# Optimization experiments

Hardware: AMD Instinct MI355X
Metric: run time of the kernel (lower is better)

The kernel has to match this reference:

```python
import jax, jax.numpy as jnp
import numpy as np

# 4-bit symmetric narrow-range weight quant (Brevitas Int-WeightPerTensorFloat style)
# and 4-bit unsigned activation quant after ReLU (QuantReLU style), with
# straight-through rounding so the same code is valid for the bwd reference.

W_QMAX = 7.0    # 2**(4-1)-1, narrow range symmetric int4: [-7, 7]
A_QMAX = 15.0   # unsigned 4-bit: [0, 15]
EPS = 1e-8


def _round_ste(x):
    return x + jax.lax.stop_gradient(jnp.round(x) - x)


def quant_weight(W):
    # per-tensor scale from max abs value
    scale = jnp.max(jnp.abs(W)) / W_QMAX + EPS
    q = jnp.clip(_round_ste(W / scale), -W_QMAX, W_QMAX)
    return q * scale


def quant_relu(x, scale):
    # ReLU fused with unsigned 4-bit quant/dequant, per-tensor learned scale
    q = jnp.clip(_round_ste(jax.nn.relu(x) / scale), 0.0, A_QMAX)
    return q * scale


def setup_inputs() -> dict:
    key = jax.random.key(0)
    k = jax.random.split(key, 4)
    B = 65536
    x = jax.random.normal(k[0], (B, 28, 28), dtype=jnp.float32)
    W1 = jax.random.normal(k[1], (512, 784), dtype=jnp.float32) * 0.05
    W2 = jax.random.normal(k[2], (512, 512), dtype=jnp.float32) * 0.05
    W3 = jax.random.normal(k[3], (10, 512), dtype=jnp.float32) * 0.05
    s1 = jnp.float32(1.0)  # QuantReLU activation scales (learned params)
    s2 = jnp.float32(1.0)
    return {"x": x, "W1": W1, "W2": W2, "W3": W3, "s1": s1, "s2": s2}


def reference(x, W1, W2, W3, s1, s2):
    h = x.reshape(x.shape[0], -1)                       # flatten [B, 784]
    h = h @ quant_weight(W1).T                          # QuantLinear 784->512
    h = quant_relu(h, s1)                               # QuantReLU
    h = h @ quant_weight(W2).T                          # QuantLinear 512->512
    h = quant_relu(h, s2)                               # QuantReLU
    logits = h @ quant_weight(W3).T                     # QuantLinear 512->10
    return logits
```

## Files before the change

### kernel.cpp

```cpp
#include <hip/hip_runtime.h>
#include <hip/hip_fp16.h>

typedef _Float16 f16;
typedef _Float16 f16x4 __attribute__((ext_vector_type(4)));
typedef _Float16 f16x8 __attribute__((ext_vector_type(8)));
typedef float f32x4 __attribute__((ext_vector_type(4)));
typedef int i32x4 __attribute__((ext_vector_type(4)));

#define MFMA16(a, b, c) __builtin_amdgcn_mfma_f32_16x16x32_f16((a), (b), (c), 0, 0, 0)
#define MFMAI8(a, b, c) __builtin_amdgcn_mfma_i32_16x16x64_i8((a), (b), (c), 0, 0, 0)

#define FLAG_CAP (1024 * 1024)
#define FLAG_TOL 1e-3f

#define SBAR()   __builtin_amdgcn_s_barrier()
#define SCHEDB() __builtin_amdgcn_sched_barrier(0)

__device__ __forceinline__ void gld16(const void* g, void* l) {
    __builtin_amdgcn_global_load_lds(
        (const __attribute__((address_space(1))) unsigned int*)g,
        (__attribute__((address_space(3))) unsigned int*)l,
        16, 0, 0);
}


__global__ void k_zero(float* p, int* cnt) {
    if (threadIdx.x < 3) p[threadIdx.x] = 0.f;
    if (threadIdx.x == 3) { cnt[0] = 0; cnt[1] = 0; }
}

__global__ void k_absmax(const float* __restrict__ w, int n, float* __restrict__ out) {
    float m = 0.f;
    int stride = gridDim.x * blockDim.x;
    for (int i = blockIdx.x * blockDim.x + threadIdx.x; i < n; i += stride)
        m = fmaxf(m, fabsf(w[i]));
    #pragma unroll
    for (int o = 32; o > 0; o >>= 1) m = fmaxf(m, __shfl_down(m, o));
    __shared__ float sm[4];
    int lane = threadIdx.x & 63, wv = threadIdx.x >> 6;
    if (lane == 0) sm[wv] = m;
    __syncthreads();
    if (threadIdx.x == 0) {
        float mm = fmaxf(fmaxf(sm[0], sm[1]), fmaxf(sm[2], sm[3]));
        atomicMax((unsigned int*)out, __float_as_uint(mm));
    }
}

__global__ void k_quantw1(const float* __restrict__ w, const float* __restrict__ wmax,
                          float* __restrict__ wdq, f16* __restrict__ q1h) {
    int i = blockIdx.x * blockDim.x + threadIdx.x;
    if (i >= 512 * 832) return;
    int n = i / 832, k = i - n * 832;
    float v = 0.f;
    if (k < 784) {
        float s = wmax[0] / 7.0f + 1e-8f;
        v = rintf(w[n * 784 + k] / s);
        v = fminf(fmaxf(v, -7.f), 7.f);
        wdq[n * 784 + k] = v * s;
    }
    q1h[(size_t)n * 832 + k] = (f16)v;
}

__global__ void k_quantw2(const float* __restrict__ w, const float* __restrict__ wmax,
                          signed char* __restrict__ q, float* __restrict__ wdq, int n) {
    float s = wmax[0] / 7.0f + 1e-8f;
    int i = blockIdx.x * blockDim.x + threadIdx.x;
    if (i < n) {
        float v = rintf(w[i] / s);
        v = fminf(fmaxf(v, -7.f), 7.f);
        q[i] = (signed char)v;
        if (wdq) wdq[i] = v * s;
    }
}

__global__ void k_quantw3(const float* __restrict__ w, const float* __restrict__ wmax,
                          signed char* __restrict__ q) {
    float s = wmax[0] / 7.0f + 1e-8f;
    int i = blockIdx.x * blockDim.x + threadIdx.x;
    if (i < 16 * 512) {
        float v = 0.f;
        if (i < 10 * 512) {
            v = rintf(w[i] / s);
            v = fminf(fmaxf(v, -7.f), 7.f);
        }
        q[i] = (signed char)v;
    }
}


__global__ __launch_bounds__(512, 2) void k_gemm1F(
    const float* __restrict__ X, const f16* __restrict__ B,
    const float* __restrict__ wmax, const float* __restrict__ s1p,
    signed char* __restrict__ A1, int* __restrict__ flagCnt, unsigned* __restrict__ flagList)
{
    constexpr int NT = 13;
    __shared__ __align__(16) f16 Ah[2][128 * 64];
    __shared__ __align__(16) f16 Al[2][128 * 64];
    __shared__ __align__(16) f16 Bt[512 * 64];

    const int t = threadIdx.x;
    const int lane = t & 63, w = t >> 6;
    const int wr = w >> 2, wc = w & 3;
    const int l15 = lane & 15, l4 = lane >> 4;
    const int row0 = blockIdx.x * 128;

    f32x4 acc[4][8];
    #pragma unroll
    for (int m = 0; m < 4; ++m)
        #pragma unroll
        for (int n = 0; n < 8; ++n) acc[m][n] = (f32x4){0.f, 0.f, 0.f, 0.f};

    const int lr = lane >> 3;
    const int lc = ((lane & 7) ^ lr) * 8;
    const f16* Bb = B + (size_t)lr * 832 + lc;

    float4 av[4];
    auto LOADA = [&](int tn) {
        #pragma unroll
        for (int i = 0; i < 4; ++i) {
            int f = t + 512 * i;
            int r = f >> 4, s = f & 15;
            int gk = tn * 64 + s * 4;
            av[i] = make_float4(0.f, 0.f, 0.f, 0.f);
            if (gk < 784)
                av[i] = *reinterpret_cast<const float4*>(X + (size_t)(row0 + r) * 784 + gk);
        }
    };
    auto WRITEA = [&](int buf) {
        #pragma unroll
        for (int i = 0; i < 4; ++i) {
            int f = t + 512 * i;
            int r = f >> 4, s = f & 15;
            float vv[4] = {av[i].x, av[i].y, av[i].z, av[i].w};
            f16x4 h0, h1;
            #pragma unroll
            for (int j = 0; j < 4; ++j) {
                f16 c0 = (f16)vv[j];
                h0[j] = c0;
                h1[j] = (f16)(vv[j] - (float)c0);
            }
            int ad = r * 64 + ((s * 4) ^ ((r & 7) << 3));
            *reinterpret_cast<f16x4*>(&Ah[buf][ad]) = h0;
            *reinterpret_cast<f16x4*>(&Al[buf][ad]) = h1;
        }
    };

    LOADA(0);
    asm volatile("s_waitcnt vmcnt(0)" ::: "memory");
    WRITEA(0);

    int cur = 0;
    for (int tt = 0; tt < NT; ++tt) {
        #pragma unroll
        for (int i = 0; i < 8; ++i) {
            int ch = w * 8 + i;
            gld16(Bb + (size_t)ch * 8 * 832 + tt * 64, &Bt[ch * 512]);
        }
        SCHEDB();
        int tn = (tt + 1 < NT) ? tt + 1 : tt;
        LOADA(tn);
        SCHEDB();
        asm volatile("s_waitcnt vmcnt(4)" ::: "memory");
        asm volatile("s_waitcnt lgkmcnt(0)" ::: "memory");
        SBAR();

        #pragma unroll
        for (int kk = 0; kk < 2; ++kk) {
            int kb = kk * 32 + l4 * 8;
            int ksw = kb ^ ((lane & 7) << 3);
            f16x8 fh[4], fl_[4], bf[8];
            #pragma unroll
            for (int m = 0; m < 4; ++m) {
                fh[m]  = *reinterpret_cast<const f16x8*>(&Ah[cur][(wr * 64 + m * 16 + l15) * 64 + ksw]);
                fl_[m] = *reinterpret_cast<const f16x8*>(&Al[cur][(wr * 64 + m * 16 + l15) * 64 + ksw]);
            }
            #pragma unroll
            for (int n = 0; n < 8; ++n)
                bf[n] = *reinterpret_cast<const f16x8*>(&Bt[(wc * 128 + n * 16 + l15) * 64 + ksw]);
            #pragma unroll
            for (int m = 0; m < 4; ++m)
                #pragma unroll
                for (int n = 0; n < 8; ++n) {
                    acc[m][n] = MFMA16(fh[m],  bf[n], acc[m][n]);
                    acc[m][n] = MFMA16(fl_[m], bf[n], acc[m][n]);
                }
        }

        asm volatile("s_waitcnt vmcnt(0)" ::: "memory");
        WRITEA(cur ^ 1);
        SBAR();
        cur ^= 1;
    }

    float sw = wmax[0] / 7.0f + 1e-8f;
    float s1v = s1p[0];
    #pragma unroll
    for (int m = 0; m < 4; ++m)
        #pragma unroll
        for (int n = 0; n < 8; ++n)
            #pragma unroll
            for (int j = 0; j < 4; ++j) {
                int row = row0 + wr * 64 + m * 16 + l4 * 4 + j;
                int col = wc * 128 + n * 16 + l15;
                float h = sw * acc[m][n][j];
                float r = fmaxf(h, 0.f) / s1v;
                float qv = fminf(rintf(r), 15.f);
                A1[(size_t)row * 512 + col] = (signed char)qv;
                float fr = r - floorf(r);
                if (fabsf(fr - 0.5f) < FLAG_TOL) {
                    int p = atomicAdd(flagCnt, 1);
                    if (p < FLAG_CAP) flagList[p] = (unsigned)(row * 512 + col);
                }
            }
}


__global__ __launch_bounds__(512, 2) void k_gemm2F(
    const signed char* __restrict__ A, const signed char* __restrict__ B,
    const float* __restrict__ wmax, const float* __restrict__ s1p, const float* __restrict__ s2p,
    signed char* __restrict__ A2, int* __restrict__ flagCnt, unsigned* __restrict__ flagList)
{
    constexpr int NT = 4;
    __shared__ __align__(16) signed char As[2][128 * 128];
    __shared__ __align__(16) signed char Bs[512 * 128];

    const int t = threadIdx.x;
    const int lane = t & 63, w = t >> 6;
    const int wr = w >> 2, wc = w & 3;
    const int l15 = lane & 15, l4 = lane >> 4;
    const int row0 = blockIdx.x * 128;

    i32x4 acc[4][8];
    #pragma unroll
    for (int m = 0; m < 4; ++m)
        #pragma unroll
        for (int n = 0; n < 8; ++n) acc[m][n] = (i32x4){0, 0, 0, 0};

    const int lr = lane >> 3;
    const int lcb = ((lane & 7) ^ lr) * 16;
    const signed char* Ab = A + (size_t)(row0 + lr) * 512 + lcb;
    const signed char* Bb = B + (size_t)lr * 512 + lcb;

    #pragma unroll
    for (int i = 0; i < 2; ++i) {
        int ch = w * 2 + i;
        gld16(Ab + (size_t)ch * 8 * 512, &As[0][ch * 1024]);
    }

    int cur = 0;
    for (int tt = 0; tt < NT; ++tt) {
        #pragma unroll
        for (int i = 0; i < 8; ++i) {
            int ch = w * 8 + i;
            gld16(Bb + (size_t)ch * 8 * 512 + tt * 128, &Bs[ch * 1024]);
        }
        SCHEDB();
        int tn = (tt + 1 < NT) ? tt + 1 : tt;
        #pragma unroll
        for (int i = 0; i < 2; ++i) {
            int ch = w * 2 + i;
            gld16(Ab + (size_t)ch * 8 * 512 + tn * 128, &As[cur ^ 1][ch * 1024]);
        }
        SCHEDB();
        asm volatile("s_waitcnt vmcnt(2)" ::: "memory");
        SBAR();

        #pragma unroll
        for (int kk = 0; kk < 2; ++kk) {
            int sl = kk * 4 + l4;
            int slw = (sl ^ (lane & 7)) * 16;
            i32x4 af[4], bf[8];
            #pragma unroll
            for (int m = 0; m < 4; ++m)
                af[m] = *reinterpret_cast<const i32x4*>(&As[cur][(wr * 64 + m * 16 + l15) * 128 + slw]);
            #pragma unroll
            for (int n = 0; n < 8; ++n)
                bf[n] = *reinterpret_cast<const i32x4*>(&Bs[(wc * 128 + n * 16 + l15) * 128 + slw]);
            #pragma unroll
            for (int m = 0; m < 4; ++m)
                #pragma unroll
                for (int n = 0; n < 8; ++n)
                    acc[m][n] = MFMAI8(af[m], bf[n], acc[m][n]);
        }

        SBAR();
        cur ^= 1;
    }

    double cs = (double)s1p[0] * (double)(wmax[0] / 7.0f + 1e-8f);
    double s2v = (double)s2p[0];
    #pragma unroll
    for (int m = 0; m < 4; ++m)
        #pragma unroll
        for (int n = 0; n < 8; ++n)
            #pragma unroll
            for (int j = 0; j < 4; ++j) {
                int row = row0 + wr * 64 + m * 16 + l4 * 4 + j;
                int col = wc * 128 + n * 16 + l15;
                double r = fmax((double)acc[m][n][j] * cs, 0.0) / s2v;
                double qv = fmin(rint(r), 15.0);
                A2[(size_t)row * 512 + col] = (signed char)qv;
                double fr = r - floor(r);
                if (fabs(fr - 0.5) < (double)FLAG_TOL && r < 16.0) {
                    int p = atomicAdd(flagCnt, 1);
                    if (p < FLAG_CAP) flagList[p] = (unsigned)(row * 512 + col);
                }
            }
}


__global__ void k_fixup1(const float* __restrict__ X, const float* __restrict__ W1dq,
                         const float* __restrict__ s1p,
                         const int* __restrict__ flagCnt, const unsigned* __restrict__ flagList,
                         signed char* __restrict__ A1)
{
    int tid = blockIdx.x * blockDim.x + threadIdx.x;
    int nthr = gridDim.x * blockDim.x;
    int n = flagCnt[0];
    if (n > FLAG_CAP) n = FLAG_CAP;
    float s1 = s1p[0];
    for (int i = tid; i < n; i += nthr) {
        unsigned idx = flagList[i];
        int row = (int)(idx >> 9), col = (int)(idx & 511);
        const float* xr = X + (size_t)row * 784;
        const float* wr = W1dq + (size_t)col * 784;
        float acc = 0.f;
        for (int k = 0; k < 784; ++k)
            acc = fmaf(xr[k], wr[k], acc);
        float tq = fmaxf(acc, 0.f) / s1;
        float code = fminf(rintf(tq), 15.f);
        A1[(size_t)row * 512 + col] = (signed char)code;
    }
}

__global__ void k_fixup2(const signed char* __restrict__ A1, const float* __restrict__ W2dq,
                         const float* __restrict__ s1p, const float* __restrict__ s2p,
                         const int* __restrict__ flagCnt, const unsigned* __restrict__ flagList,
                         signed char* __restrict__ A2)
{
    int tid = blockIdx.x * blockDim.x + threadIdx.x;
    int nthr = gridDim.x * blockDim.x;
    int n = flagCnt[0];
    if (n > FLAG_CAP) n = FLAG_CAP;
    float s1 = s1p[0], s2 = s2p[0];
    for (int i = tid; i < n; i += nthr) {
        unsigned idx = flagList[i];
        int row = (int)(idx >> 9), col = (int)(idx & 511);
        const signed char* ar = A1 + (size_t)row * 512;
        const float* wr = W2dq + (size_t)col * 512;
        float acc = 0.f;
        for (int k = 0; k < 512; ++k) {
            float adq = (float)ar[k] * s1;
            acc = fmaf(adq, wr[k], acc);
        }
        float tq = fmaxf(acc, 0.f) / s2;
        float code = fminf(rintf(tq), 15.f);
        A2[(size_t)row * 512 + col] = (signed char)code;
    }
}


__global__ __launch_bounds__(256) void k_gemm3i(
    const signed char* __restrict__ A2, const signed char* __restrict__ Q3,
    const float* __restrict__ wmax, const float* __restrict__ s2p,
    float* __restrict__ Out)
{
    __shared__ __align__(16) signed char As[256][80];
    __shared__ __align__(16) signed char Bs[16][80];

    const int t = threadIdx.x;
    const int row0 = blockIdx.x * 256;
    const int lane = t & 63, wv = t >> 6;

    i32x4 acc[4];
    #pragma unroll
    for (int m = 0; m < 4; ++m) acc[m] = (i32x4){0, 0, 0, 0};

    for (int k0 = 0; k0 < 512; k0 += 64) {
        #pragma unroll
        for (int i = 0; i < 4; ++i) {
            int f = t + 256 * i;
            int r = f >> 2, c = f & 3;
            *reinterpret_cast<uint4*>(&As[r][c * 16]) =
                *reinterpret_cast<const uint4*>(A2 + (size_t)(row0 + r) * 512 + k0 + c * 16);
        }
        if (t < 64) {
            int r = t >> 2, c = t & 3;
            *reinterpret_cast<uint4*>(&Bs[r][c * 16]) =
                *reinterpret_cast<const uint4*>(Q3 + (size_t)r * 512 + k0 + c * 16);
        }
        __syncthreads();

        i32x4 bf = *reinterpret_cast<const i32x4*>(&Bs[lane & 15][(lane >> 4) * 16]);
        #pragma unroll
        for (int m = 0; m < 4; ++m) {
            i32x4 af = *reinterpret_cast<const i32x4*>(&As[wv * 64 + m * 16 + (lane & 15)][(lane >> 4) * 16]);
            acc[m] = MFMAI8(af, bf, acc[m]);
        }
        __syncthreads();
    }

    double cs = (double)s2p[0] * (double)(wmax[0] / 7.0f + 1e-8f);
    #pragma unroll
    for (int m = 0; m < 4; ++m)
        #pragma unroll
        for (int j = 0; j < 4; ++j) {
            int row = row0 + wv * 64 + m * 16 + (lane >> 4) * 4 + j;
            int col = lane & 15;
            if (col < 10)
                Out[(size_t)row * 10 + col] = (float)((double)acc[m][j] * cs);
        }
}


extern "C" void kernel_launch(void* const* d_in, const int* in_sizes, int n_in,
                              void* d_out, int out_size, void* d_ws, size_t ws_size,
                              hipStream_t stream)
{
    (void)in_sizes; (void)n_in; (void)out_size; (void)ws_size;

    const float* X  = (const float*)d_in[0];
    const float* W1 = (const float*)d_in[1];
    const float* W2 = (const float*)d_in[2];
    const float* W3 = (const float*)d_in[3];
    const float* s1 = (const float*)d_in[4];
    const float* s2 = (const float*)d_in[5];
    float* Out = (float*)d_out;

    char* ws = (char*)d_ws;
    float* maxes     = (float*)ws;
    int*   cnts      = (int*)(ws + 16);
    f16*   q1h       = (f16*)(ws + (size_t)(1u << 20));
    float* w1dq      = (float*)(ws + (size_t)(2u << 20));
    float* w2dq      = (float*)(ws + (size_t)(4u << 20));
    signed char* q2i = (signed char*)(ws + (size_t)(6u << 20));
    signed char* q3i = (signed char*)(ws + (size_t)(6u << 20) + 300000);
    signed char* a1  = (signed char*)(ws + (size_t)(8u << 20));
    signed char* a2  = (signed char*)(ws + (size_t)(40u << 20));
    unsigned* fl1    = (unsigned*)(ws + (size_t)(72u << 20));
    unsigned* fl2    = (unsigned*)(ws + (size_t)(76u << 20));

    k_zero<<<1, 64, 0, stream>>>(maxes, cnts);
    k_absmax<<<256, 256, 0, stream>>>(W1, 512 * 784, maxes + 0);
    k_absmax<<<256, 256, 0, stream>>>(W2, 512 * 512, maxes + 1);
    k_absmax<<<8, 256, 0, stream>>>(W3, 10 * 512, maxes + 2);
    k_quantw1<<<(512 * 832 + 255) / 256, 256, 0, stream>>>(W1, maxes + 0, w1dq, q1h);
    k_quantw2<<<(512 * 512 + 255) / 256, 256, 0, stream>>>(W2, maxes + 1, q2i, w2dq, 512 * 512);
    k_quantw3<<<(16 * 512 + 255) / 256, 256, 0, stream>>>(W3, maxes + 2, q3i);

    k_gemm1F<<<512, 512, 0, stream>>>(X, q1h, maxes + 0, s1, a1, cnts + 0, fl1);
    k_fixup1<<<512, 256, 0, stream>>>(X, w1dq, s1, cnts + 0, fl1, a1);
    k_gemm2F<<<512, 512, 0, stream>>>(a1, q2i, maxes + 1, s1, s2, a2, cnts + 1, fl2);
    k_fixup2<<<512, 256, 0, stream>>>(a1, w2dq, s1, s2, cnts + 1, fl2, a2);
    k_gemm3i<<<256, 256, 0, stream>>>(a2, q3i, maxes + 2, s2, Out);
}
```

Baseline: 624.4 us.

## Restructure gemm1 with K-tile 32, double-buffered B and single-buffered A

Rewrites the first GEMM's main loop to use a 32-wide K step over 26 iterations instead of 64 over 13. The B tile is now double-buffered through direct global-to-LDS loads, while the split-fp16 A tile is single-buffered and uses a new swizzle. LDS use drops, and the launch bound is raised to ask for 4 blocks per CU, aiming at more occupancy and better overlap. The risk is that the tighter register budget forces spills of the 128-float accumulator, and the halved K step doubles barrier overhead per unit of work.

```diff
diff --git a/kernel.cpp b/kernel.cpp
--- a/kernel.cpp
+++ b/kernel.cpp
@@ -88,15 +88,15 @@
 }
 
 
-__global__ __launch_bounds__(512, 2) void k_gemm1F(
+__global__ __launch_bounds__(512, 4) void k_gemm1G(
     const float* __restrict__ X, const f16* __restrict__ B,
     const float* __restrict__ wmax, const float* __restrict__ s1p,
     signed char* __restrict__ A1, int* __restrict__ flagCnt, unsigned* __restrict__ flagList)
 {
-    constexpr int NT = 13;
-    __shared__ __align__(16) f16 Ah[2][128 * 64];
-    __shared__ __align__(16) f16 Al[2][128 * 64];
-    __shared__ __align__(16) f16 Bt[512 * 64];
+    constexpr int NT = 26;
+    __shared__ __align__(16) f16 Bt[2][512 * 32];
+    __shared__ __align__(16) f16 Ah[128 * 32];
+    __shared__ __align__(16) f16 Al[128 * 32];
 
     const int t = threadIdx.x;
     const int lane = t & 63, w = t >> 6;
@@ -110,27 +110,27 @@
         #pragma unroll
         for (int n = 0; n < 8; ++n) acc[m][n] = (f32x4){0.f, 0.f, 0.f, 0.f};
 
-    const int lr = lane >> 3;
-    const int lc = ((lane & 7) ^ lr) * 8;
-    const f16* Bb = B + (size_t)lr * 832 + lc;
-
-    float4 av[4];
+    const int blr = lane >> 2;
+    const int bslot = (lane & 3) ^ ((lane >> 3) & 3);
+    const f16* Bb = B + (size_t)blr * 832 + bslot * 8;
+
+    float4 av[2];
     auto LOADA = [&](int tn) {
         #pragma unroll
-        for (int i = 0; i < 4; ++i) {
+        for (int i = 0; i < 2; ++i) {
             int f = t + 512 * i;
-            int r = f >> 4, s = f & 15;
-            int gk = tn * 64 + s * 4;
+            int r = f >> 3, s = f & 7;
+            int gk = tn * 32 + s * 4;
             av[i] = make_float4(0.f, 0.f, 0.f, 0.f);
             if (gk < 784)
                 av[i] = *reinterpret_cast<const float4*>(X + (size_t)(row0 + r) * 784 + gk);
         }
     };
-    auto WRITEA = [&](int buf) {
-        #pragma unroll
-        for (int i = 0; i < 4; ++i) {
+    auto WRITEA = [&]() {
+        #pragma unroll
+        for (int i = 0; i < 2; ++i) {
             int f = t + 512 * i;
-            int r = f >> 4, s = f & 15;
+            int r = f >> 3, s = f & 7;
             float vv[4] = {av[i].x, av[i].y, av[i].z, av[i].w};
             f16x4 h0, h1;
             #pragma unroll
@@ -139,44 +139,54 @@
                 h0[j] = c0;
                 h1[j] = (f16)(vv[j] - (float)c0);
             }
-            int ad = r * 64 + ((s * 4) ^ ((r & 7) << 3));
-            *reinterpret_cast<f16x4*>(&Ah[buf][ad]) = h0;
-            *reinterpret_cast<f16x4*>(&Al[buf][ad]) = h1;
+            int slot = (s >> 1) ^ ((r >> 1) & 3);
+            int ad = r * 32 + slot * 8 + (s & 1) * 4;
+            *reinterpret_cast<f16x4*>(&Ah[ad]) = h0;
+            *reinterpret_cast<f16x4*>(&Al[ad]) = h1;
         }
     };
 
-    LOADA(0);
-    asm volatile("s_waitcnt vmcnt(0)" ::: "memory");
-    WRITEA(0);
+    {
+        #pragma unroll
+        for (int i = 0; i < 4; ++i) {
+            int ch = w * 4 + i;
+            gld16(Bb + (size_t)ch * 16 * 832, &Bt[0][ch * 512]);
+        }
+        LOADA(0);
+    }
 
     int cur = 0;
     for (int tt = 0; tt < NT; ++tt) {
-        #pragma unroll
-        for (int i = 0; i < 8; ++i) {
-            int ch = w * 8 + i;
-            gld16(Bb + (size_t)ch * 8 * 832 + tt * 64, &Bt[ch * 512]);
+        asm volatile("s_waitcnt vmcnt(0)" ::: "memory");
+        SBAR();
+        WRITEA();
+        if (tt + 1 < NT) {
+            #pragma unroll
+            for (int i = 0; i < 4; ++i) {
+                int ch = w * 4 + i;
+                gld16(Bb + (size_t)ch * 16 * 832 + (tt + 1) * 32, &Bt[cur ^ 1][ch * 512]);
+            }
+            LOADA(tt + 1);
         }
         SCHEDB();
-        int tn = (tt + 1 < NT) ? tt + 1 : tt;
-        LOADA(tn);
-        SCHEDB();
-        asm volatile("s_waitcnt vmcnt(4)" ::: "memory");
         asm volatile("s_waitcnt lgkmcnt(0)" ::: "memory");
         SBAR();
 
-        #pragma unroll
-        for (int kk = 0; kk < 2; ++kk) {
-            int kb = kk * 32 + l4 * 8;
-            int ksw = kb ^ ((lane & 7) << 3);
+        {
             f16x8 fh[4], fl_[4], bf[8];
             #pragma unroll
             for (int m = 0; m < 4; ++m) {
-                fh[m]  = *reinterpret_cast<const f16x8*>(&Ah[cur][(wr * 64 + m * 16 + l15) * 64 + ksw]);
-                fl_[m] = *reinterpret_cast<const f16x8*>(&Al[cur][(wr * 64 + m * 16 + l15) * 64 + ksw]);
-            }
-            #pragma unroll
-            for (int n = 0; n < 8; ++n)
-                bf[n] = *reinterpret_cast<const f16x8*>(&Bt[(wc * 128 + n * 16 + l15) * 64 + ksw]);
+                int row = wr * 64 + m * 16 + l15;
+                int ad = row * 32 + ((l4 ^ ((row >> 1) & 3)) * 8);
+                fh[m]  = *reinterpret_cast<const f16x8*>(&Ah[ad]);
+                fl_[m] = *reinterpret_cast<const f16x8*>(&Al[ad]);
+            }
+            #pragma unroll
+            for (int n = 0; n < 8; ++n) {
+                int row = wc * 128 + n * 16 + l15;
+                int ad = row * 32 + ((l4 ^ ((row >> 1) & 3)) * 8);
+                bf[n] = *reinterpret_cast<const f16x8*>(&Bt[cur][ad]);
+            }
             #pragma unroll
             for (int m = 0; m < 4; ++m)
                 #pragma unroll
@@ -185,10 +195,6 @@
                     acc[m][n] = MFMA16(fl_[m], bf[n], acc[m][n]);
                 }
         }
-
-        asm volatile("s_waitcnt vmcnt(0)" ::: "memory");
-        WRITEA(cur ^ 1);
-        SBAR();
         cur ^= 1;
     }
 
@@ -448,7 +454,7 @@
     k_quantw2<<<(512 * 512 + 255) / 256, 256, 0, stream>>>(W2, maxes + 1, q2i, w2dq, 512 * 512);
     k_quantw3<<<(16 * 512 + 255) / 256, 256, 0, stream>>>(W3, maxes + 2, q3i);
 
-    k_gemm1F<<<512, 512, 0, stream>>>(X, q1h, maxes + 0, s1, a1, cnts + 0, fl1);
+    k_gemm1G<<<512, 512, 0, stream>>>(X, q1h, maxes + 0, s1, a1, cnts + 0, fl1);
     k_fixup1<<<512, 256, 0, stream>>>(X, w1dq, s1, cnts + 0, fl1, a1);
     k_gemm2F<<<512, 512, 0, stream>>>(a1, q2i, maxes + 1, s1, s2, a2, cnts + 1, fl2);
     k_fixup2<<<512, 256, 0, stream>>>(a1, w2dq, s1, s2, cnts + 1, fl2, a2);
```

Result: slower. 1.253 ms (+100.6%).

## Replace LDS-staged GEMM1 with direct register-loaded per-wave tiles

Applied to the files above, without the earlier changes.

Rewrites the first GEMM so each wave loads its A (fp32 input, split into hi/lo fp16) and B fragments straight from global memory into registers. It double-buffers them in registers instead of staging through shared memory with barriers. Block tile shrinks to 64 rows and the grid doubles. This removes LDS traffic and barrier sync, but B is no longer shared across waves, which increases global/L2 load traffic and uses less coalesced access patterns.

```diff
diff --git a/kernel.cpp b/kernel.cpp
--- a/kernel.cpp
+++ b/kernel.cpp
@@ -88,120 +88,89 @@
 }
 
 
-__global__ __launch_bounds__(512, 2) void k_gemm1F(
+__global__ __launch_bounds__(512) void k_gemm1W(
     const float* __restrict__ X, const f16* __restrict__ B,
     const float* __restrict__ wmax, const float* __restrict__ s1p,
     signed char* __restrict__ A1, int* __restrict__ flagCnt, unsigned* __restrict__ flagList)
 {
-    constexpr int NT = 13;
-    __shared__ __align__(16) f16 Ah[2][128 * 64];
-    __shared__ __align__(16) f16 Al[2][128 * 64];
-    __shared__ __align__(16) f16 Bt[512 * 64];
-
+    constexpr int NT = 25;
     const int t = threadIdx.x;
     const int lane = t & 63, w = t >> 6;
-    const int wr = w >> 2, wc = w & 3;
     const int l15 = lane & 15, l4 = lane >> 4;
-    const int row0 = blockIdx.x * 128;
-
-    f32x4 acc[4][8];
-    #pragma unroll
-    for (int m = 0; m < 4; ++m)
+    const int row0 = blockIdx.x * 64 + (w >> 2) * 32;
+    const int col0 = (w & 3) * 128;
+
+    f32x4 acc[2][8];
+    #pragma unroll
+    for (int m = 0; m < 2; ++m)
         #pragma unroll
         for (int n = 0; n < 8; ++n) acc[m][n] = (f32x4){0.f, 0.f, 0.f, 0.f};
 
-    const int lr = lane >> 3;
-    const int lc = ((lane & 7) ^ lr) * 8;
-    const f16* Bb = B + (size_t)lr * 832 + lc;
-
-    float4 av[4];
-    auto LOADA = [&](int tn) {
-        #pragma unroll
-        for (int i = 0; i < 4; ++i) {
-            int f = t + 512 * i;
-            int r = f >> 4, s = f & 15;
-            int gk = tn * 64 + s * 4;
-            av[i] = make_float4(0.f, 0.f, 0.f, 0.f);
-            if (gk < 784)
-                av[i] = *reinterpret_cast<const float4*>(X + (size_t)(row0 + r) * 784 + gk);
-        }
+    const float* Xb = X + (size_t)(row0 + l15) * 784 + l4 * 8;
+    const f16*   Bb = B + (size_t)(col0 + l15) * 832 + l4 * 8;
+
+    struct Set { float4 x[2][2]; f16x8 b[8]; };
+    Set s0, s1;
+
+    auto LOAD = [&](Set& s, int k0) {
+        #pragma unroll
+        for (int m = 0; m < 2; ++m)
+            #pragma unroll
+            for (int i = 0; i < 2; ++i) {
+                int gk = k0 + l4 * 8 + i * 4;
+                s.x[m][i] = make_float4(0.f, 0.f, 0.f, 0.f);
+                if (gk < 784)
+                    s.x[m][i] = *reinterpret_cast<const float4*>(
+                        Xb + (size_t)m * 16 * 784 + k0 + i * 4);
+            }
+        #pragma unroll
+        for (int n = 0; n < 8; ++n)
+            s.b[n] = *reinterpret_cast<const f16x8*>(Bb + (size_t)n * 16 * 832 + k0);
     };
-    auto WRITEA = [&](int buf) {
-        #pragma unroll
-        for (int i = 0; i < 4; ++i) {
-            int f = t + 512 * i;
-            int r = f >> 4, s = f & 15;
-            float vv[4] = {av[i].x, av[i].y, av[i].z, av[i].w};
-            f16x4 h0, h1;
-            #pragma unroll
-            for (int j = 0; j < 4; ++j) {
-                f16 c0 = (f16)vv[j];
-                h0[j] = c0;
-                h1[j] = (f16)(vv[j] - (float)c0);
+
+    auto COMP = [&](Set& s) {
+        f16x8 ah[2], al[2];
+        #pragma unroll
+        for (int m = 0; m < 2; ++m)
+            #pragma unroll
+            for (int i = 0; i < 2; ++i) {
+                float vv[4] = {s.x[m][i].x, s.x[m][i].y, s.x[m][i].z, s.x[m][i].w};
+                #pragma unroll
+                for (int j = 0; j < 4; ++j) {
+                    f16 c0 = (f16)vv[j];
+                    ah[m][i * 4 + j] = c0;
+                    al[m][i * 4 + j] = (f16)(vv[j] - (float)c0);
+                }
             }
-            int ad = r * 64 + ((s * 4) ^ ((r & 7) << 3));
-            *reinterpret_cast<f16x4*>(&Ah[buf][ad]) = h0;
-            *reinterpret_cast<f16x4*>(&Al[buf][ad]) = h1;
-        }
+        #pragma unroll
+        for (int m = 0; m < 2; ++m)
+            #pragma unroll
+            for (int n = 0; n < 8; ++n) {
+                acc[m][n] = MFMA16(ah[m], s.b[n], acc[m][n]);
+                acc[m][n] = MFMA16(al[m], s.b[n], acc[m][n]);
+            }
     };
 
-    LOADA(0);
-    asm volatile("s_waitcnt vmcnt(0)" ::: "memory");
-    WRITEA(0);
-
-    int cur = 0;
-    for (int tt = 0; tt < NT; ++tt) {
-        #pragma unroll
-        for (int i = 0; i < 8; ++i) {
-            int ch = w * 8 + i;
-            gld16(Bb + (size_t)ch * 8 * 832 + tt * 64, &Bt[ch * 512]);
-        }
-        SCHEDB();
-        int tn = (tt + 1 < NT) ? tt + 1 : tt;
-        LOADA(tn);
-        SCHEDB();
-        asm volatile("s_waitcnt vmcnt(4)" ::: "memory");
-        asm volatile("s_waitcnt lgkmcnt(0)" ::: "memory");
-        SBAR();
-
-        #pragma unroll
-        for (int kk = 0; kk < 2; ++kk) {
-            int kb = kk * 32 + l4 * 8;
-            int ksw = kb ^ ((lane & 7) << 3);
-            f16x8 fh[4], fl_[4], bf[8];
-            #pragma unroll
-            for (int m = 0; m < 4; ++m) {
-                fh[m]  = *reinterpret_cast<const f16x8*>(&Ah[cur][(wr * 64 + m * 16 + l15) * 64 + ksw]);
-                fl_[m] = *reinterpret_cast<const f16x8*>(&Al[cur][(wr * 64 + m * 16 + l15) * 64 + ksw]);
-            }
-            #pragma unroll
-            for (int n = 0; n < 8; ++n)
-                bf[n] = *reinterpret_cast<const f16x8*>(&Bt[(wc * 128 + n * 16 + l15) * 64 + ksw]);
-            #pragma unroll
-            for (int m = 0; m < 4; ++m)
-                #pragma unroll
-                for (int n = 0; n < 8; ++n) {
-                    acc[m][n] = MFMA16(fh[m],  bf[n], acc[m][n]);
-                    acc[m][n] = MFMA16(fl_[m], bf[n], acc[m][n]);
-                }
-        }
-
-        asm volatile("s_waitcnt vmcnt(0)" ::: "memory");
-        WRITEA(cur ^ 1);
-        SBAR();
-        cur ^= 1;
-    }
+    LOAD(s0, 0);
+    int tt = 0;
+    for (; tt + 2 < NT; tt += 2) {
+        LOAD(s1, (tt + 1) * 32);
+        COMP(s0);
+        LOAD(s0, (tt + 2) * 32);
+        COMP(s1);
+    }
+    COMP(s0);
 
     float sw = wmax[0] / 7.0f + 1e-8f;
     float s1v = s1p[0];
     #pragma unroll
-    for (int m = 0; m < 4; ++m)
+    for (int m = 0; m < 2; ++m)
         #pragma unroll
         for (int n = 0; n < 8; ++n)
             #pragma unroll
             for (int j = 0; j < 4; ++j) {
-                int row = row0 + wr * 64 + m * 16 + l4 * 4 + j;
-                int col = wc * 128 + n * 16 + l15;
+                int row = row0 + m * 16 + l4 * 4 + j;
+                int col = col0 + n * 16 + l15;
                 float h = sw * acc[m][n][j];
                 float r = fmaxf(h, 0.f) / s1v;
                 float qv = fminf(rintf(r), 15.f);
@@ -448,7 +417,7 @@
     k_quantw2<<<(512 * 512 + 255) / 256, 256, 0, stream>>>(W2, maxes + 1, q2i, w2dq, 512 * 512);
     k_quantw3<<<(16 * 512 + 255) / 256, 256, 0, stream>>>(W3, maxes + 2, q3i);
 
-    k_gemm1F<<<512, 512, 0, stream>>>(X, q1h, maxes + 0, s1, a1, cnts + 0, fl1);
+    k_gemm1W<<<1024, 512, 0, stream>>>(X, q1h, maxes + 0, s1, a1, cnts + 0, fl1);
     k_fixup1<<<512, 256, 0, stream>>>(X, w1dq, s1, cnts + 0, fl1, a1);
     k_gemm2F<<<512, 512, 0, stream>>>(a1, q2i, maxes + 1, s1, s2, a2, cnts + 1, fl2);
     k_fixup2<<<512, 256, 0, stream>>>(a1, w2dq, s1, s2, cnts + 1, fl2, a2);
```

Result: no change. 617.2 us (-1.2%).
